# Performance work log

Hardware: AMD Instinct MI355X
Metric: run time of the kernel (lower is better)

Reference implementation:

```python
import jax, jax.numpy as jnp
import numpy as np

N = 100000   # nodes
E = 1600000  # edges
H = 128      # hidden_dim
B = 4096     # number of root pairs
HOPS = 3


def setup_inputs() -> dict:
    key = jax.random.key(0)
    ks = jax.random.split(key, 12)
    s = 0.05
    return {
        "node_feat": jax.random.normal(ks[0], (N, H), jnp.float32),
        "send_embd": jax.random.normal(ks[1], (N, H), jnp.float32),
        "edge_index": jax.random.randint(ks[2], (2, E), 0, N, dtype=jnp.int32),
        "root_index": jax.random.randint(ks[3], (2 * B,), 0, N, dtype=jnp.int32),
        "agg_by_source": 1,
        "lin1_W": jax.random.normal(ks[4], (2 * H, H), jnp.float32) * s,
        "lin1_b": jnp.zeros((H,), jnp.float32),
        "gat_W": jax.random.normal(ks[5], (HOPS, H, H), jnp.float32) * s,
        "gat_asrc": jax.random.normal(ks[6], (HOPS, H), jnp.float32) * s,
        "gat_adst": jax.random.normal(ks[7], (HOPS, H), jnp.float32) * s,
        "gat_b": jnp.zeros((HOPS, H), jnp.float32),
        "lstm_Wih": jax.random.normal(ks[8], (HOPS, 2 * H, 4 * H), jnp.float32) * s,
        "lstm_Whh": jax.random.normal(ks[9], (HOPS, H, 4 * H), jnp.float32) * s,
        "lstm_b": jnp.zeros((HOPS, 4 * H), jnp.float32),
        "lin2_W": jax.random.normal(ks[10], (H, H), jnp.float32) * s,
        "lin2_b": jnp.zeros((H,), jnp.float32),
    }


def _gat_breadth(x, src, dst, W, a_src, a_dst, b):
    # GATConv(heads=1) followed by tanh (GeniePath Breadth layer)
    xw = x @ W                                  # [N, H]
    e_score = jax.nn.leaky_relu((xw @ a_src)[src] + (xw @ a_dst)[dst], 0.2)  # [E]
    # softmax over incoming edges of each destination node
    m = jax.ops.segment_max(e_score, dst, num_segments=N)
    ex = jnp.exp(e_score - m[dst])
    z = jax.ops.segment_sum(ex, dst, num_segments=N)
    alpha = ex / z[dst]                          # [E]
    agg = jax.ops.segment_sum(alpha[:, None] * xw[src], dst, num_segments=N)
    return jnp.tanh(agg + b)


def _lstm_step(inp, h, c, Wih, Whh, b):
    gates = inp @ Wih + h @ Whh + b              # [N, 4H]
    i, f, g, o = jnp.split(gates, 4, axis=-1)
    c = jax.nn.sigmoid(f) * c + jax.nn.sigmoid(i) * jnp.tanh(g)
    h = jax.nn.sigmoid(o) * jnp.tanh(c)
    return h, c


def reference(node_feat, send_embd, edge_index, root_index, agg_by_source,
              lin1_W, lin1_b, gat_W, gat_asrc, gat_adst, gat_b,
              lstm_Wih, lstm_Whh, lstm_b, lin2_W, lin2_b):
    src, dst = edge_index[0], edge_index[1]
    # Aggregation stage input: concat node embedding with broadcast embedding
    x = jnp.concatenate([node_feat, send_embd], axis=1) @ lin1_W + lin1_b  # [N, H]
    # GeniePathLazy: all breadth (GAT) layers run on the projected input x
    h_tmps = [
        _gat_breadth(x, src, dst, gat_W[i], gat_asrc[i], gat_adst[i], gat_b[i])
        for i in range(HOPS)
    ]
    # Depth: per-node LSTM over the hop axis, input = cat(h_tmp, x_prev)
    h = jnp.zeros_like(x)
    c = jnp.zeros_like(x)
    xs = x
    for i in range(HOPS):
        inp = jnp.concatenate([h_tmps[i], xs], axis=1)   # [N, 2H]
        h, c = _lstm_step(inp, h, c, lstm_Wih[i], lstm_Whh[i], lstm_b[i])
        xs = h
    out = xs @ lin2_W + lin2_b                            # [N, H]
    roots = root_index.reshape(-1, 2)
    src_nodes = roots[:, 0] if agg_by_source else roots[:, 1]
    return out[src_nodes]                                 # [B, H]
```

## Files before the change

kernel.cpp:

```cpp
#include <hip/hip_runtime.h>

constexpr int N  = 100000;
constexpr int E  = 1600000;
constexpr int H  = 128;
constexpr int NB = 4096;
constexpr int HOPS = 3;

constexpr int WOFF_L1  = 0;
constexpr int WOFF_GAT = 32768;
constexpr int WOFF_CAT = 81920;
constexpr int WOFF_L2  = 671744;
constexpr int WTOT     = 688128;

constexpr size_t ALIGN = 256;
constexpr size_t alup(size_t x) { return (x + ALIGN - 1) & ~(ALIGN - 1); }

constexpr size_t OFF_X       = 0;
constexpr size_t OFF_SSRC    = alup(OFF_X + (size_t)N * H * 4);
constexpr size_t OFF_SDST    = alup(OFF_SSRC + (size_t)3 * N * 4);
constexpr size_t OFF_WVEC    = alup(OFF_SDST + (size_t)3 * N * 4);
constexpr size_t OFF_SELMAP  = alup(OFF_WVEC + 6 * H * 4);
constexpr size_t OFF_NODELST = alup(OFF_SELMAP + (size_t)N * 4);
constexpr size_t OFF_CNT     = alup(OFF_NODELST + NB * 4);
constexpr size_t OFF_DEG     = alup(OFF_CNT + 256);
constexpr size_t OFF_OFFS    = alup(OFF_DEG + NB * 4);
constexpr size_t OFF_CURSOR  = alup(OFF_OFFS + (NB + 1) * 4);
constexpr size_t OFF_ESORT   = alup(OFF_CURSOR + NB * 4);
constexpr size_t OFF_AGGXH   = alup(OFF_ESORT + (size_t)E * 4);
constexpr size_t OFF_AGGXL   = alup(OFF_AGGXH + (size_t)3 * NB * H * 2);
constexpr size_t OFF_XSH     = alup(OFF_AGGXL + (size_t)3 * NB * H * 2);
constexpr size_t OFF_XSL     = alup(OFF_XSH + (size_t)NB * H * 2);
constexpr size_t OFF_HH      = alup(OFF_XSL + (size_t)NB * H * 2);
constexpr size_t OFF_HL      = alup(OFF_HH + (size_t)NB * H * 2);
constexpr size_t OFF_CBUF    = alup(OFF_HL + (size_t)NB * H * 2);
constexpr size_t OFF_L2OUT   = alup(OFF_CBUF + (size_t)NB * H * 4);
constexpr size_t OFF_WHI     = alup(OFF_L2OUT + (size_t)NB * H * 4);
constexpr size_t OFF_WLO     = alup(OFF_WHI + (size_t)WTOT * 2);

__device__ __forceinline__ float lrelu(float v) { return v > 0.f ? v : 0.2f * v; }
__device__ __forceinline__ float sigmoidf_(float v) { return 1.f / (1.f + __expf(-v)); }

__device__ __forceinline__ unsigned short f2bf(float f) {
  unsigned u = __float_as_uint(f);
  unsigned r = (u + 0x7FFFu + ((u >> 16) & 1u)) >> 16;
  return (unsigned short)r;
}
__device__ __forceinline__ float bf2f(unsigned short h) {
  return __uint_as_float((unsigned)h << 16);
}
__device__ __forceinline__ void split_rne(float f, unsigned short& hi, unsigned short& lo) {
  unsigned short hh = f2bf(f);
  hi = hh;
  lo = f2bf(f - bf2f(hh));
}
__device__ __forceinline__ void split_trunc(float f, short* hi, short* lo) {
  unsigned u = __float_as_uint(f);
  *hi = (short)(u >> 16);
  float r = f - __uint_as_float(u & 0xFFFF0000u);
  *lo = (short)(__float_as_uint(r) >> 16);
}

typedef short bf16x8 __attribute__((ext_vector_type(8)));
typedef float f32x4  __attribute__((ext_vector_type(4)));

#define MFMA3(ACC, AH, AL, BH, BL)                                               \
  ACC = __builtin_amdgcn_mfma_f32_16x16x32_bf16(AH, BH, ACC, 0, 0, 0);           \
  ACC = __builtin_amdgcn_mfma_f32_16x16x32_bf16(AH, BL, ACC, 0, 0, 0);           \
  ACC = __builtin_amdgcn_mfma_f32_16x16x32_bf16(AL, BH, ACC, 0, 0, 0);

__global__ void init_ws(int* __restrict__ sel_map, int* __restrict__ deg,
                        int* __restrict__ cursor, int* __restrict__ cnt,
                        float* __restrict__ cbuf, unsigned short* __restrict__ hh,
                        unsigned short* __restrict__ hl) {
  int i = blockIdx.x * 256 + threadIdx.x;
  int stride = gridDim.x * 256;
  for (int n = i; n < N; n += stride) sel_map[n] = -1;
  for (int n = i; n < NB; n += stride) { deg[n] = 0; cursor[n] = 0; }
  if (i < 64) cnt[i] = 0;
  for (int n = i; n < NB * H; n += stride) { cbuf[n] = 0.f; hh[n] = 0; hl[n] = 0; }
}

__global__ void prep_kernel(const float* __restrict__ gat_W,
                            const float* __restrict__ a_src,
                            const float* __restrict__ a_dst,
                            float* __restrict__ wvec,
                            const float* __restrict__ lin1_W,
                            const float* __restrict__ Wih,
                            const float* __restrict__ Whh,
                            const float* __restrict__ lin2_W,
                            unsigned short* __restrict__ whi,
                            unsigned short* __restrict__ wlo) {
  if (blockIdx.x < 6) {
    int i = blockIdx.x >> 1, which = blockIdx.x & 1;
    int k = threadIdx.x;
    __shared__ float av[H];
    if (k < H) av[k] = which ? a_dst[i * H + k] : a_src[i * H + k];
    __syncthreads();
    if (k >= H) return;
    const float* Wr = gat_W + (size_t)i * H * H + (size_t)k * H;
    float s = 0.f;
    #pragma unroll 8
    for (int j = 0; j < H; j++) s = fmaf(Wr[j], av[j], s);
    wvec[(i * 2 + which) * H + k] = s;
    return;
  }
  int idx = (blockIdx.x - 6) * 256 + threadIdx.x;
  if (idx >= WTOT) return;
  float v;
  if (idx < WOFF_GAT) {
    int rel = idx;
    int e = rel & 7, lane = (rel >> 3) & 63, tile = rel >> 9;
    int nl = lane & 15, quad = lane >> 4;
    int c = tile & 7, t = tile >> 3;
    int n = c * 16 + nl, k = t * 32 + quad * 8 + e;
    v = lin1_W[k * 128 + n];
  } else if (idx < WOFF_CAT) {
    int rel = idx - WOFF_GAT;
    int hop = rel / 16384; rel %= 16384;
    int e = rel & 7, lane = (rel >> 3) & 63, tile = rel >> 9;
    int nl = lane & 15, quad = lane >> 4;
    int c = tile & 7, t = tile >> 3;
    int n = c * 16 + nl, k = t * 32 + quad * 8 + e;
    v = gat_W[hop * 16384 + k * 128 + n];
  } else if (idx < WOFF_L2) {
    int rel = idx - WOFF_CAT;
    int hop = rel / 196608; rel %= 196608;
    int e = rel & 7, lane = (rel >> 3) & 63, tile = rel >> 9;
    int nl = lane & 15, quad = lane >> 4;
    int c = tile & 31, t = tile >> 5;
    int ftile = c >> 2, g = c & 3;
    int col = g * 128 + ftile * 16 + nl;
    int k = t * 32 + quad * 8 + e;
    v = (k < 256) ? Wih[hop * 131072 + k * 512 + col]
                  : Whh[hop * 65536 + (k - 256) * 512 + col];
  } else {
    int rel = idx - WOFF_L2;
    int e = rel & 7, lane = (rel >> 3) & 63, tile = rel >> 9;
    int nl = lane & 15, quad = lane >> 4;
    int c = tile & 7, t = tile >> 3;
    int n = c * 16 + nl, k = t * 32 + quad * 8 + e;
    v = lin2_W[k * 128 + n];
  }
  unsigned short hh, ll;
  split_rne(v, hh, ll);
  whi[idx] = hh;
  wlo[idx] = ll;
}

__global__ void roots_assign(const int* __restrict__ root, const int* __restrict__ aggp,
                             int* __restrict__ sel_map, int* __restrict__ node_list,
                             int* __restrict__ cnt) {
  int b = blockIdx.x * 256 + threadIdx.x;
  if (b >= NB) return;
  int node = root[2 * b + (aggp[0] ? 0 : 1)];
  int old = atomicCAS(&sel_map[node], -1, -2);
  if (old == -1) {
    int c = atomicAdd(cnt, 1);
    sel_map[node] = c;
    node_list[c] = node;
  }
}

__global__ __launch_bounds__(256)
void gemm_lin1(const float* __restrict__ a0, const float* __restrict__ a1,
               const unsigned short* __restrict__ Bth,
               const unsigned short* __restrict__ Btl,
               const float* __restrict__ bias, float* __restrict__ Cc,
               const float* __restrict__ wvec,
               float* __restrict__ s_src, float* __restrict__ s_dst, int M) {
  const int t = threadIdx.x, lane = t & 63, wave = t >> 6;
  const int nl = lane & 15, quad = lane >> 4;
  const int rt = blockIdx.x * 128 + wave * 32;

  f32x4 acc[2][8];
  #pragma unroll
  for (int i = 0; i < 2; i++)
    #pragma unroll
    for (int c = 0; c < 8; c++) acc[i][c] = (f32x4){0.f, 0.f, 0.f, 0.f};

  #pragma unroll
  for (int kt = 0; kt < 8; kt++) {
    const float* A = (kt < 4) ? a0 : a1;
    const int kk = (kt & 3) * 32 + quad * 8;
    bf16x8 ahi[2], alo[2];
    #pragma unroll
    for (int i = 0; i < 2; i++) {
      int row = rt + i * 16 + nl;
      float4 v0 = make_float4(0.f, 0.f, 0.f, 0.f), v1 = v0;
      if (row < M) {
        const float* p = A + (size_t)row * H + kk;
        v0 = *(const float4*)p;
        v1 = *(const float4*)(p + 4);
      }
      float af[8] = {v0.x, v0.y, v0.z, v0.w, v1.x, v1.y, v1.z, v1.w};
      #pragma unroll
      for (int j = 0; j < 8; j++) {
        short h_, l_;
        split_trunc(af[j], &h_, &l_);
        ahi[i][j] = h_;
        alo[i][j] = l_;
      }
    }
    #pragma unroll
    for (int c = 0; c < 8; c++) {
      size_t boff = ((size_t)(kt * 8 + c) * 64 + lane) * 8;
      bf16x8 bh = *(const bf16x8*)(Bth + boff);
      bf16x8 bl = *(const bf16x8*)(Btl + boff);
      #pragma unroll
      for (int i = 0; i < 2; i++) { MFMA3(acc[i][c], ahi[i], alo[i], bh, bl); }
    }
  }

  float bv[8], wvf[6][8];
  #pragma unroll
  for (int c = 0; c < 8; c++) {
    int col = c * 16 + nl;
    bv[c] = bias[col];
    #pragma unroll
    for (int v6 = 0; v6 < 6; v6++) wvf[v6][c] = wvec[v6 * 128 + col];
  }
  #pragma unroll
  for (int i = 0; i < 2; i++)
    #pragma unroll
    for (int r = 0; r < 4; r++) {
      int row = rt + i * 16 + quad * 4 + r;
      if (row >= M) continue;
      float* cr = Cc + (size_t)row * H;
      float sc[6] = {0.f, 0.f, 0.f, 0.f, 0.f, 0.f};
      #pragma unroll
      for (int c = 0; c < 8; c++) {
        float val = acc[i][c][r] + bv[c];
        cr[c * 16 + nl] = val;
        #pragma unroll
        for (int v6 = 0; v6 < 6; v6++) sc[v6] = fmaf(val, wvf[v6][c], sc[v6]);
      }
      #pragma unroll
      for (int m = 1; m < 16; m <<= 1)
        #pragma unroll
        for (int v6 = 0; v6 < 6; v6++) sc[v6] += __shfl_xor(sc[v6], m);
      if (nl == 0) {
        #pragma unroll
        for (int h3 = 0; h3 < 3; h3++) {
          s_src[h3 * N + row] = sc[2 * h3 + 0];
          s_dst[h3 * N + row] = sc[2 * h3 + 1];
        }
      }
    }
}

__global__ void count_edges(const int* __restrict__ ei, const int* __restrict__ sel_map,
                            int* __restrict__ deg) {
  int e = blockIdx.x * 256 + threadIdx.x;
  if (e >= E) return;
  int d = sel_map[ei[E + e]];
  if (d >= 0) atomicAdd(&deg[d], 1);
}

__global__ __launch_bounds__(1024)
void scan_kernel(const int* __restrict__ deg, int* __restrict__ offs) {
  __shared__ int part[1024];
  int t = threadIdx.x;
  int base = t * 4;
  int v0 = deg[base], v1 = deg[base + 1], v2 = deg[base + 2], v3 = deg[base + 3];
  int s = v0 + v1 + v2 + v3;
  part[t] = s;
  __syncthreads();
  for (int off = 1; off < 1024; off <<= 1) {
    int tmp = (t >= off) ? part[t - off] : 0;
    __syncthreads();
    part[t] += tmp;
    __syncthreads();
  }
  int run = part[t] - s;
  offs[base] = run; run += v0;
  offs[base + 1] = run; run += v1;
  offs[base + 2] = run; run += v2;
  offs[base + 3] = run; run += v3;
  if (t == 1023) offs[NB] = part[1023];
}

__global__ void scatter_edges2(const int* __restrict__ ei, const int* __restrict__ sel_map,
                               const int* __restrict__ offs, int* __restrict__ cursor,
                               int* __restrict__ es_sorted) {
  int e = blockIdx.x * 256 + threadIdx.x;
  if (e >= E) return;
  int d = sel_map[ei[E + e]];
  if (d >= 0) {
    int p = atomicAdd(&cursor[d], 1);
    es_sorted[offs[d] + p] = ei[e];
  }
}

__global__ __launch_bounds__(128)
void gat_node_kernel(const int* __restrict__ node_list, const int* __restrict__ cntp,
                     const int* __restrict__ offs, const int* __restrict__ es_sorted,
                     const float* __restrict__ x, const float* __restrict__ s_src,
                     const float* __restrict__ s_dst,
                     unsigned short* __restrict__ aggxh, unsigned short* __restrict__ aggxl,
                     unsigned short* __restrict__ xsh, unsigned short* __restrict__ xsl) {
  int c = blockIdx.x;
  if (c >= cntp[0]) return;
  int t = threadIdx.x;
  int n = node_list[c];
  {
    float xv = x[(size_t)n * H + t];
    unsigned short vh, vl;
    split_rne(xv, vh, vl);
    xsh[(size_t)c * H + t] = vh;
    xsl[(size_t)c * H + t] = vl;
  }
  float sd0 = s_dst[0 * N + n], sd1 = s_dst[1 * N + n], sd2 = s_dst[2 * N + n];
  int e0 = offs[c], e1 = offs[c + 1];
  float m0 = -1e30f, m1 = -1e30f, m2 = -1e30f;
  for (int e = e0 + t; e < e1; e += 128) {
    int s = es_sorted[e];
    m0 = fmaxf(m0, lrelu(s_src[0 * N + s] + sd0));
    m1 = fmaxf(m1, lrelu(s_src[1 * N + s] + sd1));
    m2 = fmaxf(m2, lrelu(s_src[2 * N + s] + sd2));
  }
  __shared__ float red[3][128];
  red[0][t] = m0; red[1][t] = m1; red[2][t] = m2;
  __syncthreads();
  for (int s2 = 64; s2 > 0; s2 >>= 1) {
    if (t < s2) {
      red[0][t] = fmaxf(red[0][t], red[0][t + s2]);
      red[1][t] = fmaxf(red[1][t], red[1][t + s2]);
      red[2][t] = fmaxf(red[2][t], red[2][t + s2]);
    }
    __syncthreads();
  }
  m0 = red[0][0]; m1 = red[1][0]; m2 = red[2][0];
  float u0 = 0.f, u1 = 0.f, u2 = 0.f, z0 = 0.f, z1 = 0.f, z2 = 0.f;
  for (int e = e0; e < e1; e++) {
    int s = es_sorted[e];
    float xs = x[(size_t)s * H + t];
    float ex0 = __expf(lrelu(s_src[0 * N + s] + sd0) - m0);
    float ex1 = __expf(lrelu(s_src[1 * N + s] + sd1) - m1);
    float ex2 = __expf(lrelu(s_src[2 * N + s] + sd2) - m2);
    z0 += ex0; z1 += ex1; z2 += ex2;
    u0 = fmaf(ex0, xs, u0); u1 = fmaf(ex1, xs, u1); u2 = fmaf(ex2, xs, u2);
  }
  size_t cb = (size_t)c * H + t;
  bool any = e1 > e0;
  float v0 = any ? u0 / z0 : 0.f;
  float v1 = any ? u1 / z1 : 0.f;
  float v2 = any ? u2 / z2 : 0.f;
  unsigned short vh, vl;
  split_rne(v0, vh, vl); aggxh[0 * ((size_t)NB * H) + cb] = vh; aggxl[0 * ((size_t)NB * H) + cb] = vl;
  split_rne(v1, vh, vl); aggxh[1 * ((size_t)NB * H) + cb] = vh; aggxl[1 * ((size_t)NB * H) + cb] = vl;
  split_rne(v2, vh, vl); aggxh[2 * ((size_t)NB * H) + cb] = vh; aggxl[2 * ((size_t)NB * H) + cb] = vl;
}

__global__ __launch_bounds__(256)
void hop_fused(const unsigned short* __restrict__ agh, const unsigned short* __restrict__ agl,
               const unsigned short* __restrict__ gWh, const unsigned short* __restrict__ gWl,
               const float* __restrict__ gbias,
               const unsigned short* __restrict__ x1h, const unsigned short* __restrict__ x1l,
               const unsigned short* __restrict__ CWh, const unsigned short* __restrict__ CWl,
               const float* __restrict__ lbias,
               float* __restrict__ cbuf, unsigned short* __restrict__ hh,
               unsigned short* __restrict__ hl,
               const unsigned short* __restrict__ L2h, const unsigned short* __restrict__ L2l,
               const float* __restrict__ lin2_b, float* __restrict__ l2out, int do_lin2) {
  __shared__ unsigned short Hh[16 * 136];
  __shared__ unsigned short Hl[16 * 136];
  const int t = threadIdx.x, lane = t & 63, wave = t >> 6;
  const int nl = lane & 15, quad = lane >> 4;
  const int r0 = blockIdx.x * 16;

  f32x4 acc1[2];
  #pragma unroll
  for (int j = 0; j < 2; j++) acc1[j] = (f32x4){0.f, 0.f, 0.f, 0.f};
  #pragma unroll
  for (int kt = 0; kt < 4; kt++) {
    size_t aoff = (size_t)(r0 + nl) * H + kt * 32 + quad * 8;
    bf16x8 ah = *(const bf16x8*)(agh + aoff);
    bf16x8 al = *(const bf16x8*)(agl + aoff);
    #pragma unroll
    for (int j = 0; j < 2; j++) {
      size_t boff = ((size_t)(kt * 8 + 2 * wave + j) * 64 + lane) * 8;
      bf16x8 bh = *(const bf16x8*)(gWh + boff);
      bf16x8 bl = *(const bf16x8*)(gWl + boff);
      MFMA3(acc1[j], ah, al, bh, bl);
    }
  }
  #pragma unroll
  for (int j = 0; j < 2; j++) {
    int col = wave * 32 + j * 16 + nl;
    float bv = gbias[col];
    #pragma unroll
    for (int r = 0; r < 4; r++) {
      int rl = quad * 4 + r;
      float v = tanhf(acc1[j][r] + bv);
      unsigned short vh, vl2;
      split_rne(v, vh, vl2);
      Hh[rl * 136 + col] = vh;
      Hl[rl * 136 + col] = vl2;
    }
  }
  __syncthreads();

  f32x4 acc2[8];
  #pragma unroll
  for (int j = 0; j < 8; j++) acc2[j] = (f32x4){0.f, 0.f, 0.f, 0.f};
  for (int kt = 0; kt < 12; kt++) {
    int kk = (kt & 3) * 32 + quad * 8;
    bf16x8 ah, al;
    if (kt < 4) {
      ah = *(const bf16x8*)&Hh[nl * 136 + kk];
      al = *(const bf16x8*)&Hl[nl * 136 + kk];
    } else {
      const unsigned short* ph = (kt < 8) ? x1h : hh;
      const unsigned short* pl = (kt < 8) ? x1l : hl;
      size_t aoff = (size_t)(r0 + nl) * H + kk;
      ah = *(const bf16x8*)(ph + aoff);
      al = *(const bf16x8*)(pl + aoff);
    }
    #pragma unroll
    for (int cc = 0; cc < 8; cc++) {
      size_t boff = ((size_t)(kt * 32 + 8 * wave + cc) * 64 + lane) * 8;
      bf16x8 bh = *(const bf16x8*)(CWh + boff);
      bf16x8 bl = *(const bf16x8*)(CWl + boff);
      MFMA3(acc2[cc], ah, al, bh, bl);
    }
  }
  __syncthreads();

  #pragma unroll
  for (int ft = 0; ft < 2; ft++) {
    int f = (2 * wave + ft) * 16 + nl;
    float b_i = lbias[0 * 128 + f], b_f = lbias[1 * 128 + f];
    float b_g = lbias[2 * 128 + f], b_o = lbias[3 * 128 + f];
    #pragma unroll
    for (int r = 0; r < 4; r++) {
      int rl = quad * 4 + r;
      size_t id = (size_t)(r0 + rl) * H + f;
      float gi = acc2[ft * 4 + 0][r] + b_i;
      float gf = acc2[ft * 4 + 1][r] + b_f;
      float gg = acc2[ft * 4 + 2][r] + b_g;
      float go = acc2[ft * 4 + 3][r] + b_o;
      float cp = cbuf[id];
      float cn = sigmoidf_(gf) * cp + sigmoidf_(gi) * tanhf(gg);
      float hn = sigmoidf_(go) * tanhf(cn);
      cbuf[id] = cn;
      unsigned short vh, vl2;
      split_rne(hn, vh, vl2);
      hh[id] = vh;
      hl[id] = vl2;
      if (do_lin2) { Hh[rl * 136 + f] = vh; Hl[rl * 136 + f] = vl2; }
    }
  }

  if (!do_lin2) return;
  __syncthreads();
  f32x4 acc3[2];
  #pragma unroll
  for (int j = 0; j < 2; j++) acc3[j] = (f32x4){0.f, 0.f, 0.f, 0.f};
  #pragma unroll
  for (int kt = 0; kt < 4; kt++) {
    int kk = kt * 32 + quad * 8;
    bf16x8 ah = *(const bf16x8*)&Hh[nl * 136 + kk];
    bf16x8 al = *(const bf16x8*)&Hl[nl * 136 + kk];
    #pragma unroll
    for (int j = 0; j < 2; j++) {
      size_t boff = ((size_t)(kt * 8 + 2 * wave + j) * 64 + lane) * 8;
      bf16x8 bh = *(const bf16x8*)(L2h + boff);
      bf16x8 bl = *(const bf16x8*)(L2l + boff);
      MFMA3(acc3[j], ah, al, bh, bl);
    }
  }
  #pragma unroll
  for (int j = 0; j < 2; j++) {
    int col = wave * 32 + j * 16 + nl;
    float bv = lin2_b[col];
    #pragma unroll
    for (int r = 0; r < 4; r++) {
      int row = r0 + quad * 4 + r;
      l2out[(size_t)row * H + col] = acc3[j][r] + bv;
    }
  }
}

__global__ void scatter_out(const float* __restrict__ l2out, const int* __restrict__ sel_map,
                            const int* __restrict__ root, const int* __restrict__ aggp,
                            float* __restrict__ out) {
  int id = blockIdx.x * 256 + threadIdx.x;
  if (id >= NB * H) return;
  int b = id >> 7, f = id & 127;
  int node = root[2 * b + (aggp[0] ? 0 : 1)];
  int c = sel_map[node];
  out[id] = l2out[(size_t)c * H + f];
}

extern "C" void kernel_launch(void* const* d_in, const int* in_sizes, int n_in,
                              void* d_out, int out_size, void* d_ws, size_t ws_size,
                              hipStream_t stream) {
  const float* node_feat = (const float*)d_in[0];
  const float* send_embd = (const float*)d_in[1];
  const int*   edge_idx  = (const int*)d_in[2];
  const int*   root_idx  = (const int*)d_in[3];
  const int*   aggp      = (const int*)d_in[4];
  const float* lin1_W    = (const float*)d_in[5];
  const float* lin1_b    = (const float*)d_in[6];
  const float* gat_W     = (const float*)d_in[7];
  const float* gat_asrc  = (const float*)d_in[8];
  const float* gat_adst  = (const float*)d_in[9];
  const float* gat_b     = (const float*)d_in[10];
  const float* lstm_Wih  = (const float*)d_in[11];
  const float* lstm_Whh  = (const float*)d_in[12];
  const float* lstm_b    = (const float*)d_in[13];
  const float* lin2_W    = (const float*)d_in[14];
  const float* lin2_b    = (const float*)d_in[15];
  float* out = (float*)d_out;

  char* ws = (char*)d_ws;
  float* x       = (float*)(ws + OFF_X);
  float* s_src   = (float*)(ws + OFF_SSRC);
  float* s_dst   = (float*)(ws + OFF_SDST);
  float* wvec    = (float*)(ws + OFF_WVEC);
  int*   sel_map = (int*)(ws + OFF_SELMAP);
  int*   nodelst = (int*)(ws + OFF_NODELST);
  int*   cnt     = (int*)(ws + OFF_CNT);
  int*   deg     = (int*)(ws + OFF_DEG);
  int*   offs    = (int*)(ws + OFF_OFFS);
  int*   cursor  = (int*)(ws + OFF_CURSOR);
  int*   esort   = (int*)(ws + OFF_ESORT);
  unsigned short* aggxh = (unsigned short*)(ws + OFF_AGGXH);
  unsigned short* aggxl = (unsigned short*)(ws + OFF_AGGXL);
  unsigned short* xsh   = (unsigned short*)(ws + OFF_XSH);
  unsigned short* xsl   = (unsigned short*)(ws + OFF_XSL);
  unsigned short* hh    = (unsigned short*)(ws + OFF_HH);
  unsigned short* hl    = (unsigned short*)(ws + OFF_HL);
  float* cbuf    = (float*)(ws + OFF_CBUF);
  float* l2out   = (float*)(ws + OFF_L2OUT);
  unsigned short* whi = (unsigned short*)(ws + OFF_WHI);
  unsigned short* wlo = (unsigned short*)(ws + OFF_WLO);

  init_ws<<<2048, 256, 0, stream>>>(sel_map, deg, cursor, cnt, cbuf, hh, hl);
  prep_kernel<<<6 + (WTOT + 255) / 256, 256, 0, stream>>>(
      gat_W, gat_asrc, gat_adst, wvec, lin1_W, lstm_Wih, lstm_Whh, lin2_W, whi, wlo);
  roots_assign<<<(NB + 255) / 256, 256, 0, stream>>>(root_idx, aggp, sel_map, nodelst, cnt);

  gemm_lin1<<<(N + 127) / 128, 256, 0, stream>>>(
      node_feat, send_embd, whi + WOFF_L1, wlo + WOFF_L1, lin1_b, x,
      wvec, s_src, s_dst, N);

  count_edges<<<(E + 255) / 256, 256, 0, stream>>>(edge_idx, sel_map, deg);
  scan_kernel<<<1, 1024, 0, stream>>>(deg, offs);
  scatter_edges2<<<(E + 255) / 256, 256, 0, stream>>>(edge_idx, sel_map, offs, cursor, esort);
  gat_node_kernel<<<NB, 128, 0, stream>>>(nodelst, cnt, offs, esort, x, s_src, s_dst,
                                          aggxh, aggxl, xsh, xsl);

  for (int i = 0; i < HOPS; i++) {
    const unsigned short* x1h = (i == 0) ? xsh : hh;
    const unsigned short* x1l = (i == 0) ? xsl : hl;
    hop_fused<<<NB / 16, 256, 0, stream>>>(
        aggxh + (size_t)i * NB * H, aggxl + (size_t)i * NB * H,
        whi + WOFF_GAT + i * 16384, wlo + WOFF_GAT + i * 16384,
        gat_b + (size_t)i * H,
        x1h, x1l,
        whi + WOFF_CAT + i * 196608, wlo + WOFF_CAT + i * 196608,
        lstm_b + (size_t)i * 512,
        cbuf, hh, hl,
        whi + WOFF_L2, wlo + WOFF_L2, lin2_b, l2out,
        (i == HOPS - 1) ? 1 : 0);
  }

  scatter_out<<<(NB * H + 255) / 256, 256, 0, stream>>>(l2out, sel_map, root_idx, aggp, out);
}
```

Baseline: 378.9 us.

## Compute lin1 projection only for nodes reachable from selected roots

Builds a deduplicated list of needed nodes (the selected roots plus the sources of their incoming edges) during root assignment and edge scatter, then runs the lin1 GEMM only over those rows via indirect row indexing. The edge bucketing kernels move ahead of the GEMM so the list is ready in time. This cuts the dense lin1 GEMM over all N nodes down to the reachable subset, at the cost of extra atomics in the scatter and gathered, non-contiguous row loads. The flag and list buffers reuse the aggregation buffer space, which is safe only because that space is written later by gat_node_kernel.

After: 582.1 us. 1.54x slower.

```diff
diff --git a/kernel.cpp b/kernel.cpp
--- a/kernel.cpp
+++ b/kernel.cpp
@@ -71,10 +71,10 @@
 __global__ void init_ws(int* __restrict__ sel_map, int* __restrict__ deg,
                         int* __restrict__ cursor, int* __restrict__ cnt,
                         float* __restrict__ cbuf, unsigned short* __restrict__ hh,
-                        unsigned short* __restrict__ hl) {
+                        unsigned short* __restrict__ hl, int* __restrict__ need_flag) {
   int i = blockIdx.x * 256 + threadIdx.x;
   int stride = gridDim.x * 256;
-  for (int n = i; n < N; n += stride) sel_map[n] = -1;
+  for (int n = i; n < N; n += stride) { sel_map[n] = -1; need_flag[n] = 0; }
   for (int n = i; n < NB; n += stride) { deg[n] = 0; cursor[n] = 0; }
   if (i < 64) cnt[i] = 0;
   for (int n = i; n < NB * H; n += stride) { cbuf[n] = 0.f; hh[n] = 0; hl[n] = 0; }
@@ -149,7 +149,8 @@
 
 __global__ void roots_assign(const int* __restrict__ root, const int* __restrict__ aggp,
                              int* __restrict__ sel_map, int* __restrict__ node_list,
-                             int* __restrict__ cnt) {
+                             int* __restrict__ cnt, int* __restrict__ need_flag,
+                             int* __restrict__ need_list, int* __restrict__ need_cnt) {
   int b = blockIdx.x * 256 + threadIdx.x;
   if (b >= NB) return;
   int node = root[2 * b + (aggp[0] ? 0 : 1)];
@@ -158,6 +159,10 @@
     int c = atomicAdd(cnt, 1);
     sel_map[node] = c;
     node_list[c] = node;
+    if (atomicCAS(&need_flag[node], 0, 1) == 0) {
+      int q = atomicAdd(need_cnt, 1);
+      need_list[q] = node;
+    }
   }
 }
 
@@ -167,10 +172,20 @@
                const unsigned short* __restrict__ Btl,
                const float* __restrict__ bias, float* __restrict__ Cc,
                const float* __restrict__ wvec,
-               float* __restrict__ s_src, float* __restrict__ s_dst, int M) {
+               float* __restrict__ s_src, float* __restrict__ s_dst,
+               const int* __restrict__ need_list, const int* __restrict__ need_cnt) {
   const int t = threadIdx.x, lane = t & 63, wave = t >> 6;
   const int nl = lane & 15, quad = lane >> 4;
+  const int nneed = need_cnt[0];
+  if (blockIdx.x * 128 >= nneed) return;
   const int rt = blockIdx.x * 128 + wave * 32;
+
+  int rowi[2];
+  #pragma unroll
+  for (int i = 0; i < 2; i++) {
+    int gr = rt + i * 16 + nl;
+    rowi[i] = (gr < nneed) ? need_list[gr] : -1;
+  }
 
   f32x4 acc[2][8];
   #pragma unroll
@@ -185,9 +200,9 @@
     bf16x8 ahi[2], alo[2];
     #pragma unroll
     for (int i = 0; i < 2; i++) {
-      int row = rt + i * 16 + nl;
+      int row = rowi[i];
       float4 v0 = make_float4(0.f, 0.f, 0.f, 0.f), v1 = v0;
-      if (row < M) {
+      if (row >= 0) {
         const float* p = A + (size_t)row * H + kk;
         v0 = *(const float4*)p;
         v1 = *(const float4*)(p + 4);
@@ -223,8 +238,9 @@
   for (int i = 0; i < 2; i++)
     #pragma unroll
     for (int r = 0; r < 4; r++) {
-      int row = rt + i * 16 + quad * 4 + r;
-      if (row >= M) continue;
+      int gr = rt + i * 16 + quad * 4 + r;
+      if (gr >= nneed) continue;
+      int row = need_list[gr];
       float* cr = Cc + (size_t)row * H;
       float sc[6] = {0.f, 0.f, 0.f, 0.f, 0.f, 0.f};
       #pragma unroll
@@ -275,19 +291,25 @@
   offs[base] = run; run += v0;
   offs[base + 1] = run; run += v1;
   offs[base + 2] = run; run += v2;
-  offs[base + 3] = run; run += v3;
+  offs[base + 3] = run;
   if (t == 1023) offs[NB] = part[1023];
 }
 
 __global__ void scatter_edges2(const int* __restrict__ ei, const int* __restrict__ sel_map,
                                const int* __restrict__ offs, int* __restrict__ cursor,
-                               int* __restrict__ es_sorted) {
+                               int* __restrict__ es_sorted, int* __restrict__ need_flag,
+                               int* __restrict__ need_list, int* __restrict__ need_cnt) {
   int e = blockIdx.x * 256 + threadIdx.x;
   if (e >= E) return;
   int d = sel_map[ei[E + e]];
   if (d >= 0) {
     int p = atomicAdd(&cursor[d], 1);
-    es_sorted[offs[d] + p] = ei[e];
+    int s = ei[e];
+    es_sorted[offs[d] + p] = s;
+    if (atomicCAS(&need_flag[s], 0, 1) == 0) {
+      int q = atomicAdd(need_cnt, 1);
+      need_list[q] = s;
+    }
   }
 }
 
@@ -536,18 +558,25 @@
   unsigned short* whi = (unsigned short*)(ws + OFF_WHI);
   unsigned short* wlo = (unsigned short*)(ws + OFF_WLO);
 
-  init_ws<<<2048, 256, 0, stream>>>(sel_map, deg, cursor, cnt, cbuf, hh, hl);
+  int* need_flag = (int*)(ws + OFF_AGGXH);
+  int* need_list = need_flag + N;
+  int* need_cnt  = cnt + 1;
+
+  init_ws<<<2048, 256, 0, stream>>>(sel_map, deg, cursor, cnt, cbuf, hh, hl, need_flag);
   prep_kernel<<<6 + (WTOT + 255) / 256, 256, 0, stream>>>(
       gat_W, gat_asrc, gat_adst, wvec, lin1_W, lstm_Wih, lstm_Whh, lin2_W, whi, wlo);
-  roots_assign<<<(NB + 255) / 256, 256, 0, stream>>>(root_idx, aggp, sel_map, nodelst, cnt);
+  roots_assign<<<(NB + 255) / 256, 256, 0, stream>>>(root_idx, aggp, sel_map, nodelst, cnt,
+                                                     need_flag, need_list, need_cnt);
+
+  count_edges<<<(E + 255) / 256, 256, 0, stream>>>(edge_idx, sel_map, deg);
+  scan_kernel<<<1, 1024, 0, stream>>>(deg, offs);
+  scatter_edges2<<<(E + 255) / 256, 256, 0, stream>>>(edge_idx, sel_map, offs, cursor, esort,
+                                                      need_flag, need_list, need_cnt);
 
   gemm_lin1<<<(N + 127) / 128, 256, 0, stream>>>(
       node_feat, send_embd, whi + WOFF_L1, wlo + WOFF_L1, lin1_b, x,
-      wvec, s_src, s_dst, N);
-
-  count_edges<<<(E + 255) / 256, 256, 0, stream>>>(edge_idx, sel_map, deg);
-  scan_kernel<<<1, 1024, 0, stream>>>(deg, offs);
-  scatter_edges2<<<(E + 255) / 256, 256, 0, stream>>>(edge_idx, sel_map, offs, cursor, esort);
+      wvec, s_src, s_dst, need_list, need_cnt);
+
   gat_node_kernel<<<NB, 128, 0, stream>>>(nodelst, cnt, offs, esort, x, s_src, s_dst,
                                           aggxh, aggxl, xsh, xsl);
 
```
